# Performance work log

Hardware: AMD Instinct MI355X
Metric: run time of the kernel (lower is better)

## Reference

```python
import jax, jax.numpy as jnp
import numpy as np

NUM_TARGETS = 2
N_ITER = 20
REF_MIC = 1          # 1-based reference mic
CONTRAST = 'laplace'
GAMMA = 1.0
PROJ_BACK = 'mdp'
TOL = 1e-5
EPS_R = 1e-10
REG = 1e-6


def contrast_weights(r, func, gamma, eps_r):
    # phi(r) = g'(r) / r for the chosen contrast function
    r = jnp.maximum(r, eps_r)
    if func == 'laplace':
        return 1.0 / (2.0 * r)
    if func == 'gaussian':
        return jnp.ones_like(r)
    if func == 'power':
        return gamma * r ** (gamma - 2.0)
    raise ValueError(func)


def _iva_forward(X):
    M, T, F, _ = X.shape
    K = NUM_TARGETS
    # (M,T,F,2) real/imag -> complex (F,M,T)
    X_c = jnp.transpose(X[..., 0] + 1j * X[..., 1], (2, 0, 1))
    cdtype = X_c.dtype
    eyeM = jnp.eye(M, dtype=cdtype)
    W_hat = jnp.tile(eyeM[None], (F, 1, 1))
    W_hat = W_hat.at[:, K:, K:].set(-jnp.eye(M - K, dtype=cdtype))
    # input covariance (constant over iterations): (F,M,M)
    C = jnp.einsum('fmt,fnt->fmn', X_c, X_c.conj()) / T
    reg_eye = REG * eyeM  # broadcasts over F / (K,F)
    eps = jnp.finfo(jnp.float32).eps
    done = jnp.array(False)

    for _ in range(N_ITER):
        W_old = W_hat
        # current target estimates: (F,K,T)
        Y = jnp.einsum('fkm,fmt->fkt', W_hat[:, :K, :], X_c)
        r = jnp.sqrt(jnp.maximum((jnp.abs(Y) ** 2).sum(axis=0), EPS_R))  # (K,T)
        w_t = contrast_weights(r, CONTRAST, GAMMA, EPS_R).astype(cdtype)
        # weighted covariances: (K,F,M,M)
        V = jnp.einsum('kt,fmt,fnt->kfmn', w_t, X_c, X_c.conj()) / T
        V_reg = V + reg_eye

        Wn = W_hat
        for k in range(K):
            temp = Wn @ V_reg[k]                              # (F,M,M)
            e_k = jnp.zeros((F, M), dtype=cdtype).at[:, k].set(1.0)
            w_vec = jnp.linalg.solve(temp, e_k[..., None])[..., 0]  # (F,M)
            denom = jnp.sqrt(
                jnp.einsum('fm,fmn,fn->f', w_vec.conj(), V_reg[k], w_vec).real + EPS_R
            )
            Wn = Wn.at[:, k, :].set((w_vec / denom[:, None]).conj())
        # background block: J = solve(tmp[:, :, :K], tmp[:, :, K:])^H
        tmp = Wn[:, :K, :] @ C                                # (F,K,M)
        J = jnp.conj(jnp.swapaxes(jnp.linalg.solve(tmp[:, :, :K], tmp[:, :, K:]), 1, 2))
        Wn = Wn.at[:, K:, :K].set(J)

        rel = jnp.linalg.norm(Wn - W_old) / jnp.maximum(jnp.linalg.norm(W_old), eps)
        W_hat = jnp.where(done, W_old, Wn)  # freeze once converged (mimics break)
        done = done | (rel < TOL)

    W = W_hat[:, :K, :]
    Y = jnp.einsum('fkm,fmt->fkt', W, X_c)  # (F,K,T)
    if REF_MIC is not None and 0 < REF_MIC <= M:
        if PROJ_BACK == 'mdp':
            A = jnp.linalg.pinv(W)               # (F,M,K)
            scale = A[:, REF_MIC - 1, :]         # (F,K)
            Y = scale[:, :, None] * Y
        elif PROJ_BACK == 'scale_constraint':
            Wp = jnp.linalg.pinv(W)
            d = jnp.max(jnp.abs(Wp), axis=1)     # (F,K)
            Y = d[:, :, None].astype(cdtype) * Y
    Y_out = jnp.transpose(Y, (1, 2, 0))          # (K,T,F)
    return jnp.stack([Y_out.real, Y_out.imag], axis=-1)


def setup_inputs() -> dict:
    key = jax.random.key(0)
    X = jax.random.normal(key, (8, 2048, 513, 2), dtype=jnp.float32)
    return {"X": X}


def reference(X):
    return _iva_forward(X)
```

## Files before the change

### kernel.cpp

```cpp
#include <hip/hip_runtime.h>

#define F_ 513
#define M_ 8
#define T_ 2048
#define K_ 2
#define NITER 20
#define REGC 1e-6
#define EPSR 1e-10
#define TOLC 1e-5
#define NG 256
#define TS 4
#define UPB ((F_ + 3) / 4)

typedef double2 cd;
__device__ __forceinline__ cd cmk(double r, double i){ cd z; z.x=r; z.y=i; return z; }
__device__ __forceinline__ cd cadd(cd a, cd b){ return cmk(a.x+b.x, a.y+b.y); }
__device__ __forceinline__ cd csub(cd a, cd b){ return cmk(a.x-b.x, a.y-b.y); }
__device__ __forceinline__ cd cmul(cd a, cd b){ return cmk(a.x*b.x - a.y*b.y, a.x*b.y + a.y*b.x); }
__device__ __forceinline__ cd cconj(cd a){ return cmk(a.x, -a.y); }
__device__ __forceinline__ cd cdiv(cd a, cd b){
  double d = b.x*b.x + b.y*b.y;
  return cmk((a.x*b.x + a.y*b.y)/d, (a.y*b.x - a.x*b.y)/d);
}
__device__ __forceinline__ double cabs2(cd a){ return a.x*a.x + a.y*a.y; }
__device__ __forceinline__ cd shflc(cd v, int l){
  cd r; r.x = __shfl(v.x, l, 64); r.y = __shfl(v.y, l, 64); return r;
}
__device__ __forceinline__ cd sel8(const cd x[8], int idx){
  cd r = x[0];
  #pragma unroll
  for (int q=1;q<8;++q) if (idx==q) r = x[q];
  return r;
}

__global__ __launch_bounds__(256) void pack_kernel(const float2* __restrict__ Xin, float2* __restrict__ Xc){
  __shared__ float tr[64][65];
  __shared__ float ti[64][65];
  int f0 = blockIdx.x*64, t0 = blockIdx.y*64, m = blockIdx.z;
  for (int i = threadIdx.x; i < 64*64; i += 256){
    int tl = i >> 6, fl = i & 63;
    int f = f0 + fl;
    float2 v; v.x = 0.f; v.y = 0.f;
    if (f < F_) v = Xin[((size_t)m*T_ + (t0 + tl))*F_ + f];
    tr[tl][fl] = v.x; ti[tl][fl] = v.y;
  }
  __syncthreads();
  for (int i = threadIdx.x; i < 64*32; i += 256){
    int fl = i >> 5, tl2 = i & 31;
    int f = f0 + fl;
    if (f < F_){
      int t = 2*tl2;
      float4 v;
      v.x = tr[t][fl];   v.y = ti[t][fl];
      v.z = tr[t+1][fl]; v.w = ti[t+1][fl];
      *(float4*)&Xc[((size_t)f*8 + m)*T_ + t0 + t] = v;
    }
  }
}

__global__ __launch_bounds__(256) void winit_kernel(float2* __restrict__ W){
  int idx = blockIdx.x*256 + threadIdx.x;
  if (idx >= F_*64) return;
  int l = idx & 63; int i = l>>3, j = l&7;
  float v = (i==j) ? (i < K_ ? 1.f : -1.f) : 0.f;
  float2 o; o.x = v; o.y = 0.f;
  W[idx] = o;
}

template<int MODE>
__global__ __launch_bounds__(512, 8) void cov_kernel(const float2* __restrict__ Xc, const float2* __restrict__ wts2,
                                                     cd* __restrict__ outP, const int* __restrict__ flags){
  if (MODE == 1 && *(volatile const int*)flags) return;
  __shared__ float2 xs[8][514];
  __shared__ float2 wsm2[512];
  int f = blockIdx.x, s = blockIdx.y;
  int tid = threadIdx.x;
  int w = tid >> 6, lane = tid & 63;
  int m = lane >> 3, n = lane & 7;
  #pragma unroll
  for (int r=0; r<4; ++r){
    int idx = tid + r*512;
    int mm = idx >> 8, q = idx & 255;
    float4 v = ((const float4*)(Xc + ((size_t)f*8 + mm)*T_ + s*512))[q];
    *(float4*)&xs[mm][q*2] = v;
  }
  if (MODE == 1) wsm2[tid] = wts2[s*512 + tid];
  __syncthreads();
  const float2* xm = xs[m];
  const float2* xn = xs[n];
  int tbase = w*64;
  float a0r=0.f, a0i=0.f, a1r=0.f, a1i=0.f;
  #pragma unroll 8
  for (int tt=0; tt<64; tt+=2){
    float4 av = *(const float4*)&xm[tbase+tt];
    float4 bv = *(const float4*)&xn[tbase+tt];
    float zr0 = fmaf(av.x, bv.x, av.y*bv.y);
    float zi0 = fmaf(av.y, bv.x, -av.x*bv.y);
    float zr1 = fmaf(av.z, bv.z, av.w*bv.w);
    float zi1 = fmaf(av.w, bv.z, -av.z*bv.w);
    if (MODE == 0){
      a0r += zr0 + zr1; a0i += zi0 + zi1;
    } else {
      float4 wv = *(const float4*)&wsm2[tbase+tt];
      a0r = fmaf(wv.x, zr0, a0r); a0i = fmaf(wv.x, zi0, a0i);
      a1r = fmaf(wv.y, zr0, a1r); a1i = fmaf(wv.y, zi0, a1i);
      a0r = fmaf(wv.z, zr1, a0r); a0i = fmaf(wv.z, zi1, a0i);
      a1r = fmaf(wv.w, zr1, a1r); a1i = fmaf(wv.w, zi1, a1i);
    }
  }
  __syncthreads();
  float* wred = (float*)&xs[0][0];
  wred[0*512 + w*64 + lane] = a0r;
  wred[1*512 + w*64 + lane] = a0i;
  if (MODE == 1){
    wred[2*512 + w*64 + lane] = a1r;
    wred[3*512 + w*64 + lane] = a1i;
  }
  __syncthreads();
  const double inv = 1.0/(double)T_;
  int nk = (MODE == 0) ? 1 : 2;
  if (tid < nk*64){
    int k = tid >> 6, l = tid & 63;
    float rr = 0.f, ii = 0.f;
    #pragma unroll
    for (int ww=0; ww<8; ++ww){
      rr += wred[(k*2+0)*512 + ww*64 + l];
      ii += wred[(k*2+1)*512 + ww*64 + l];
    }
    cd o = cmk((double)rr*inv, (double)ii*inv);
    if (MODE == 0) outP[((size_t)f*TS + s)*64 + l] = o;
    else           outP[(((size_t)k*F_ + f)*TS + s)*64 + l] = o;
  }
}

__global__ __launch_bounds__(256) void yr_kernel(const float2* __restrict__ Xc, const float2* __restrict__ Wg,
                                                 float* __restrict__ part, const int* __restrict__ flags){
  if (*(volatile const int*)flags) return;
  int g = blockIdx.y;
  int t = blockIdx.x*256 + threadIdx.x;
  float acc0 = 0.f, acc1 = 0.f;
  for (int f = g; f < F_; f += NG){
    const float2* Wf = Wg + (size_t)f*64;
    float2 y0; y0.x=0; y0.y=0;
    float2 y1; y1.x=0; y1.y=0;
    #pragma unroll
    for (int m=0;m<8;++m){
      float2 xv = Xc[((size_t)f*8 + m)*T_ + t];
      float2 w0 = Wf[m];
      float2 w1 = Wf[8+m];
      y0.x = fmaf(w0.x,xv.x,fmaf(-w0.y,xv.y,y0.x)); y0.y = fmaf(w0.x,xv.y,fmaf(w0.y,xv.x,y0.y));
      y1.x = fmaf(w1.x,xv.x,fmaf(-w1.y,xv.y,y1.x)); y1.y = fmaf(w1.x,xv.y,fmaf(w1.y,xv.x,y1.y));
    }
    acc0 += y0.x*y0.x + y0.y*y0.y;
    acc1 += y1.x*y1.x + y1.y*y1.y;
  }
  part[((size_t)g*2+0)*T_ + t] = acc0;
  part[((size_t)g*2+1)*T_ + t] = acc1;
}

__global__ __launch_bounds__(256) void rw_kernel(const float* __restrict__ part, float* __restrict__ wts2f,
                                                 const int* __restrict__ flags){
  if (*(volatile const int*)flags) return;
  int v = blockIdx.x*256 + threadIdx.x;
  int k = v >> 11, t = v & (T_-1);
  double s = 0;
  for (int g=0; g<NG; ++g) s += (double)part[((size_t)g*2+k)*T_ + t];
  wts2f[2*t + k] = (float)(0.5 / sqrt(fmax(s, EPSR)));
}

__global__ __launch_bounds__(256) void update_kernel(const cd* __restrict__ Vp, const cd* __restrict__ Cp,
                                                     float2* __restrict__ Wg,
                                                     double* __restrict__ dsum, double* __restrict__ osum,
                                                     int* __restrict__ flags){
  if (*(volatile const int*)flags) return;
  int lane = threadIdx.x & 63;
  int w = threadIdx.x >> 6;
  int f = blockIdx.x*4 + w;
  int i = lane >> 3, j = lane & 7;
  double ds = 0.0, os = 0.0;
  if (f < F_){
    float2 wf = Wg[(size_t)f*64 + lane];
    cd Wn = cmk(wf.x, wf.y);
    cd Wold = Wn;
    cd x[8];
    #pragma unroll
    for (int k=0; k<K_; ++k){
      cd Vr = cmk(0,0);
      #pragma unroll
      for (int s2=0; s2<TS; ++s2)
        Vr = cadd(Vr, Vp[(((size_t)k*F_ + f)*TS + s2)*64 + lane]);
      if (i == j) Vr.x += REGC;
      cd temp = cmk(0,0);
      #pragma unroll
      for (int q=0;q<8;++q) temp = cadd(temp, cmul(shflc(Wn, i*8+q), shflc(Vr, q*8+j)));
      cd b = cmk(i==k ? 1.0 : 0.0, 0.0);
      for (int p=0; p<8; ++p){
        double pv = (j==p && i>=p) ? cabs2(temp) : -1.0;
        int pidx = i;
        for (int off=32; off; off>>=1){
          double ov = __shfl_xor(pv, off, 64);
          int oi = __shfl_xor(pidx, off, 64);
          if (ov > pv){ pv = ov; pidx = oi; }
        }
        cd tp = shflc(temp, pidx*8 + j);
        cd tq = shflc(temp, p*8 + j);
        cd bp_ = shflc(b, pidx*8 + j);
        cd bq_ = shflc(b, p*8 + j);
        if (i == p){ temp = tp; b = bp_; }
        else if (i == pidx){ temp = tq; b = bq_; }
        cd tip = shflc(temp, i*8 + p);
        cd tpp = shflc(temp, p*8 + p);
        cd tpj = shflc(temp, p*8 + j);
        cd bpr = shflc(b, p*8 + j);
        cd fac = cdiv(tip, tpp);
        if (i > p){ temp = csub(temp, cmul(fac, tpj)); b = csub(b, cmul(fac, bpr)); }
      }
      #pragma unroll
      for (int p=7; p>=0; --p){
        cd s = shflc(b, p*8);
        #pragma unroll
        for (int q=p+1; q<8; ++q){
          cd tpq = shflc(temp, p*8 + q);
          s = csub(s, cmul(tpq, x[q]));
        }
        x[p] = cdiv(s, shflc(temp, p*8 + p));
      }
      cd xi = sel8(x, i), xj = sel8(x, j);
      cd z = cmul(cconj(xi), Vr);
      double dl = z.x*xj.x - z.y*xj.y;
      for (int off=32; off; off>>=1) dl += __shfl_xor(dl, off, 64);
      double denom = sqrt(dl + EPSR);
      if (i == k){ Wn = cmk(xj.x/denom, -xj.y/denom); }
    }
    cd Cc = cmk(0,0);
    #pragma unroll
    for (int s2=0; s2<TS; ++s2)
      Cc = cadd(Cc, Cp[((size_t)f*TS + s2)*64 + lane]);
    cd tmp = cmk(0,0);
    #pragma unroll
    for (int q=0;q<8;++q) tmp = cadd(tmp, cmul(shflc(Wn, i*8+q), shflc(Cc, q*8+j)));
    cd A = shflc(tmp, 0), B = shflc(tmp, 1), C2 = shflc(tmp, 8), D = shflc(tmp, 9);
    cd det = csub(cmul(A,D), cmul(B,C2));
    cd t0 = shflc(tmp, i);
    cd t1 = shflc(tmp, 8 + i);
    cd Z0 = cdiv(csub(cmul(D,t0), cmul(B,t1)), det);
    cd Z1 = cdiv(csub(cmul(A,t1), cmul(C2,t0)), det);
    if (i >= K_ && j < K_){
      cd Z = (j==0) ? Z0 : Z1;
      Wn = cconj(Z);
    }
    ds = cabs2(csub(Wn, Wold));
    os = cabs2(Wold);
    for (int off=32; off; off>>=1){
      ds += __shfl_xor(ds, off, 64);
      os += __shfl_xor(os, off, 64);
    }
    float2 wo; wo.x = (float)Wn.x; wo.y = (float)Wn.y;
    Wg[(size_t)f*64 + lane] = wo;
  }
  __shared__ double sd[4], so[4];
  __shared__ int lastFlag;
  if (lane == 0){ sd[w] = ds; so[w] = os; }
  __syncthreads();
  if (threadIdx.x == 0){
    dsum[blockIdx.x] = sd[0]+sd[1]+sd[2]+sd[3];
    osum[blockIdx.x] = so[0]+so[1]+so[2]+so[3];
  }
  __threadfence();
  if (threadIdx.x == 0){
    int tk = atomicAdd(&flags[1], 1);
    lastFlag = (tk == UPB-1) ? 1 : 0;
  }
  __syncthreads();
  if (lastFlag && threadIdx.x < 64){
    __threadfence();
    double d=0, o=0;
    for (int idx=lane; idx<UPB; idx+=64){
      d += ((volatile double*)dsum)[idx];
      o += ((volatile double*)osum)[idx];
    }
    for (int off=32; off; off>>=1){ d += __shfl_xor(d, off, 64); o += __shfl_xor(o, off, 64); }
    if (lane == 0){
      flags[1] = 0;
      double rel = sqrt(d) / fmax(sqrt(o), 1.1920928955078125e-7);
      if (rel < TOLC) flags[0] = 1;
    }
  }
}

__global__ __launch_bounds__(256) void scale_kernel(const float2* __restrict__ Wg, float2* __restrict__ scale){
  int f = blockIdx.x*256 + threadIdx.x;
  if (f >= F_) return;
  cd w0[8], w1[8];
  #pragma unroll
  for (int m=0;m<8;++m){
    float2 a = Wg[(size_t)f*64 + m];     w0[m] = cmk(a.x, a.y);
    float2 b = Wg[(size_t)f*64 + 8 + m]; w1[m] = cmk(b.x, b.y);
  }
  cd G00 = cmk(0,0), G01 = cmk(0,0), G11 = cmk(0,0);
  #pragma unroll
  for (int m=0;m<8;++m){
    G00 = cadd(G00, cmul(w0[m], cconj(w0[m])));
    G01 = cadd(G01, cmul(w0[m], cconj(w1[m])));
    G11 = cadd(G11, cmul(w1[m], cconj(w1[m])));
  }
  cd G10 = cconj(G01);
  cd det = csub(cmul(G00,G11), cmul(G01,G10));
  cd I00 = cdiv(G11, det), I01 = cdiv(cmk(-G01.x,-G01.y), det);
  cd I10 = cdiv(cmk(-G10.x,-G10.y), det), I11 = cdiv(G00, det);
  cd c0 = cconj(w0[0]), c1 = cconj(w1[0]);
  cd s0 = cadd(cmul(c0, I00), cmul(c1, I10));
  cd s1 = cadd(cmul(c0, I01), cmul(c1, I11));
  float2 o0; o0.x=(float)s0.x; o0.y=(float)s0.y;
  float2 o1; o1.x=(float)s1.x; o1.y=(float)s1.y;
  scale[(size_t)f*2 + 0] = o0;
  scale[(size_t)f*2 + 1] = o1;
}

__global__ __launch_bounds__(256) void out_kernel(const float2* __restrict__ Xc, const float2* __restrict__ Wg,
                                                  const float2* __restrict__ scale, float2* __restrict__ out){
  __shared__ float re0[32][65], im0[32][65], re1[32][65], im1[32][65];
  int f0 = blockIdx.x*32, t0 = blockIdx.y*64;
  int lane = threadIdx.x & 63, w = threadIdx.x >> 6;
  for (int fl = w; fl < 32; fl += 4){
    int f = f0 + fl;
    if (f < F_){
      const float2* Wf = Wg + (size_t)f*64;
      int t = t0 + lane;
      float2 y0; y0.x=0; y0.y=0;
      float2 y1; y1.x=0; y1.y=0;
      #pragma unroll
      for (int m=0;m<8;++m){
        float2 xv = Xc[((size_t)f*8 + m)*T_ + t];
        float2 w0 = Wf[m];
        float2 w1 = Wf[8+m];
        y0.x += w0.x*xv.x - w0.y*xv.y; y0.y += w0.x*xv.y + w0.y*xv.x;
        y1.x += w1.x*xv.x - w1.y*xv.y; y1.y += w1.x*xv.y + w1.y*xv.x;
      }
      float2 s0 = scale[(size_t)f*2 + 0];
      float2 s1 = scale[(size_t)f*2 + 1];
      re0[fl][lane] = s0.x*y0.x - s0.y*y0.y; im0[fl][lane] = s0.x*y0.y + s0.y*y0.x;
      re1[fl][lane] = s1.x*y1.x - s1.y*y1.y; im1[fl][lane] = s1.x*y1.y + s1.y*y1.x;
    }
  }
  __syncthreads();
  for (int i = threadIdx.x; i < 32*64; i += 256){
    int tl = i >> 5, fl = i & 31;
    int f = f0 + fl;
    if (f < F_){
      int t = t0 + tl;
      float2 o0; o0.x = re0[fl][tl]; o0.y = im0[fl][tl];
      float2 o1; o1.x = re1[fl][tl]; o1.y = im1[fl][tl];
      out[((size_t)(0*T_ + t))*F_ + f] = o0;
      out[((size_t)(1*T_ + t))*F_ + f] = o1;
    }
  }
}

extern "C" void kernel_launch(void* const* d_in, const int* in_sizes, int n_in,
                              void* d_out, int out_size, void* d_ws, size_t ws_size,
                              hipStream_t stream) {
  const float2* Xin = (const float2*)d_in[0];
  char* ws = (char*)d_ws;
  size_t off = 0;
  auto alloc = [&](size_t bytes) -> void* {
    void* p = ws + off;
    off += (bytes + 255) & ~(size_t)255;
    return p;
  };
  float2* Xc   = (float2*)alloc((size_t)F_*M_*T_*8);
  cd*     Cp   = (cd*)alloc((size_t)F_*TS*64*16);
  cd*     Vp   = (cd*)alloc((size_t)K_*F_*TS*64*16);
  float2* W    = (float2*)alloc((size_t)F_*64*8);
  float*  part = (float*)alloc((size_t)NG*K_*T_*4);
  float2* wts2 = (float2*)alloc((size_t)T_*8);
  double* dsum = (double*)alloc((size_t)UPB*8);
  double* osum = (double*)alloc((size_t)UPB*8);
  float2* sc   = (float2*)alloc((size_t)F_*K_*8);
  int*    flags= (int*)alloc(256);
  if (off > ws_size) return;

  hipMemsetAsync(flags, 0, 12, stream);

  pack_kernel<<<dim3(9, 32, 8), 256, 0, stream>>>(Xin, Xc);
  winit_kernel<<<(F_*64 + 255)/256, 256, 0, stream>>>(W);
  cov_kernel<0><<<dim3(F_, TS), 512, 0, stream>>>(Xc, nullptr, Cp, flags);

  for (int it=0; it<NITER; ++it){
    yr_kernel<<<dim3(T_/256, NG), 256, 0, stream>>>(Xc, W, part, flags);
    rw_kernel<<<(K_*T_ + 255)/256, 256, 0, stream>>>(part, (float*)wts2, flags);
    cov_kernel<1><<<dim3(F_, TS), 512, 0, stream>>>(Xc, wts2, Vp, flags);
    update_kernel<<<UPB, 256, 0, stream>>>(Vp, Cp, W, dsum, osum, flags);
  }

  scale_kernel<<<(F_ + 255)/256, 256, 0, stream>>>(W, sc);
  out_kernel<<<dim3(17, 32), 256, 0, stream>>>(Xc, W, sc, (float2*)d_out);
}
```

Measured before the change: 1.670 ms.

## Fuse weighted covariance, W update and next Y-power into one per-frequency kernel

Merges the weighted covariance, the per-frequency demixing update and the next iteration's |Y|^2 computation into a single kernel with one block per frequency. This cuts the loop from four launches to two and drops the global Vp round trip. The first iteration's power is taken from cov0 because W starts as identity. The rw reduction now sums per-frequency partials over 513 entries instead of 256 groups, and the pack tile height is halved. The cost is that only 513 blocks loop serially over time segments, so parallelism falls, and one wave does the solve while the others wait.

```diff
diff --git a/kernel.cpp b/kernel.cpp
--- a/kernel.cpp
+++ b/kernel.cpp
@@ -8,9 +8,7 @@
 #define REGC 1e-6
 #define EPSR 1e-10
 #define TOLC 1e-5
-#define NG 256
 #define TS 4
-#define UPB ((F_ + 3) / 4)
 
 typedef double2 cd;
 __device__ __forceinline__ cd cmk(double r, double i){ cd z; z.x=r; z.y=i; return z; }
@@ -34,10 +32,10 @@
 }
 
 __global__ __launch_bounds__(256) void pack_kernel(const float2* __restrict__ Xin, float2* __restrict__ Xc){
-  __shared__ float tr[64][65];
-  __shared__ float ti[64][65];
-  int f0 = blockIdx.x*64, t0 = blockIdx.y*64, m = blockIdx.z;
-  for (int i = threadIdx.x; i < 64*64; i += 256){
+  __shared__ float tr[32][65];
+  __shared__ float ti[32][65];
+  int f0 = blockIdx.x*64, t0 = blockIdx.y*32, m = blockIdx.z;
+  for (int i = threadIdx.x; i < 32*64; i += 256){
     int tl = i >> 6, fl = i & 63;
     int f = f0 + fl;
     float2 v; v.x = 0.f; v.y = 0.f;
@@ -45,8 +43,8 @@
     tr[tl][fl] = v.x; ti[tl][fl] = v.y;
   }
   __syncthreads();
-  for (int i = threadIdx.x; i < 64*32; i += 256){
-    int fl = i >> 5, tl2 = i & 31;
+  for (int i = threadIdx.x; i < 64*16; i += 256){
+    int fl = i >> 4, tl2 = i & 15;
     int f = f0 + fl;
     if (f < F_){
       int t = 2*tl2;
@@ -67,12 +65,10 @@
   W[idx] = o;
 }
 
-template<int MODE>
-__global__ __launch_bounds__(512, 8) void cov_kernel(const float2* __restrict__ Xc, const float2* __restrict__ wts2,
-                                                     cd* __restrict__ outP, const int* __restrict__ flags){
-  if (MODE == 1 && *(volatile const int*)flags) return;
+__global__ __launch_bounds__(512) void cov0_kernel(const float2* __restrict__ Xc, cd* __restrict__ Cp,
+                                                   float2* __restrict__ part){
   __shared__ float2 xs[8][514];
-  __shared__ float2 wsm2[512];
+  __shared__ double wred[2][8][64];
   int f = blockIdx.x, s = blockIdx.y;
   int tid = threadIdx.x;
   int w = tid >> 6, lane = tid & 63;
@@ -84,111 +80,135 @@
     float4 v = ((const float4*)(Xc + ((size_t)f*8 + mm)*T_ + s*512))[q];
     *(float4*)&xs[mm][q*2] = v;
   }
-  if (MODE == 1) wsm2[tid] = wts2[s*512 + tid];
-  __syncthreads();
+  __syncthreads();
+  {
+    float2 x0 = xs[0][tid], x1 = xs[1][tid];
+    part[(size_t)f*T_ + s*512 + tid] =
+      make_float2(fmaf(x0.x,x0.x,x0.y*x0.y), fmaf(x1.x,x1.x,x1.y*x1.y));
+  }
   const float2* xm = xs[m];
   const float2* xn = xs[n];
   int tbase = w*64;
-  float a0r=0.f, a0i=0.f, a1r=0.f, a1i=0.f;
+  float ar=0.f, ai=0.f;
   #pragma unroll 8
   for (int tt=0; tt<64; tt+=2){
     float4 av = *(const float4*)&xm[tbase+tt];
     float4 bv = *(const float4*)&xn[tbase+tt];
-    float zr0 = fmaf(av.x, bv.x, av.y*bv.y);
-    float zi0 = fmaf(av.y, bv.x, -av.x*bv.y);
-    float zr1 = fmaf(av.z, bv.z, av.w*bv.w);
-    float zi1 = fmaf(av.w, bv.z, -av.z*bv.w);
-    if (MODE == 0){
-      a0r += zr0 + zr1; a0i += zi0 + zi1;
-    } else {
+    ar += fmaf(av.x, bv.x, av.y*bv.y) + fmaf(av.z, bv.z, av.w*bv.w);
+    ai += fmaf(av.y, bv.x, -av.x*bv.y) + fmaf(av.w, bv.z, -av.z*bv.w);
+  }
+  wred[0][w][lane] = ar; wred[1][w][lane] = ai;
+  __syncthreads();
+  if (tid < 64){
+    double sr=0, si=0;
+    #pragma unroll
+    for (int ww=0; ww<8; ++ww){ sr += wred[0][ww][tid]; si += wred[1][ww][tid]; }
+    const double inv = 1.0/(double)T_;
+    Cp[((size_t)f*TS + s)*64 + tid] = cmk(sr*inv, si*inv);
+  }
+}
+
+__global__ __launch_bounds__(512) void rw_kernel(const float2* __restrict__ part, float2* __restrict__ wts2,
+                                                 const int* __restrict__ flags){
+  if (*(volatile const int*)flags) return;
+  __shared__ double wred[8][64][2];
+  int tid = threadIdx.x;
+  int w = tid >> 6, lane = tid & 63;
+  int t = blockIdx.x*64 + lane;
+  double s0=0, s1=0;
+  for (int f=w; f<F_; f+=8){
+    float2 p = part[(size_t)f*T_ + t];
+    s0 += (double)p.x; s1 += (double)p.y;
+  }
+  wred[w][lane][0]=s0; wred[w][lane][1]=s1;
+  __syncthreads();
+  if (tid < 64){
+    double a=0,b=0;
+    #pragma unroll
+    for (int ww=0; ww<8; ++ww){ a += wred[ww][tid][0]; b += wred[ww][tid][1]; }
+    wts2[blockIdx.x*64 + tid] =
+      make_float2((float)(0.5/sqrt(fmax(a,EPSR))), (float)(0.5/sqrt(fmax(b,EPSR))));
+  }
+}
+
+__global__ __launch_bounds__(512, 4) void covupd_kernel(
+    const float2* __restrict__ Xc, const float2* __restrict__ wts2,
+    const cd* __restrict__ Cp, float2* __restrict__ Wg,
+    float2* __restrict__ part, double* __restrict__ dsum, double* __restrict__ osum,
+    int* __restrict__ flags, int do_yr)
+{
+  if (*(volatile const int*)flags) return;
+  __shared__ float2 xs[8][514];
+  __shared__ float2 wsm2[512];
+  __shared__ double wred[4][8][64];
+  __shared__ double Vd[2][64][2];
+  __shared__ cd Cl[64];
+  __shared__ cd Wl[64];
+  __shared__ int lastF;
+  int f = blockIdx.x;
+  int tid = threadIdx.x;
+  int w = tid >> 6, lane = tid & 63;
+  int m = lane >> 3, n = lane & 7;
+  double va0r=0, va0i=0, va1r=0, va1i=0;
+  for (int s=0; s<TS; ++s){
+    if (s) __syncthreads();
+    #pragma unroll
+    for (int r=0; r<4; ++r){
+      int idx = tid + r*512;
+      int mm = idx >> 8, q = idx & 255;
+      float4 v = ((const float4*)(Xc + ((size_t)f*8 + mm)*T_ + s*512))[q];
+      *(float4*)&xs[mm][q*2] = v;
+    }
+    wsm2[tid] = wts2[s*512 + tid];
+    __syncthreads();
+    const float2* xm = xs[m];
+    const float2* xn = xs[n];
+    int tbase = w*64;
+    float a0r=0.f, a0i=0.f, a1r=0.f, a1i=0.f;
+    #pragma unroll 8
+    for (int tt=0; tt<64; tt+=2){
+      float4 av = *(const float4*)&xm[tbase+tt];
+      float4 bv = *(const float4*)&xn[tbase+tt];
+      float zr0 = fmaf(av.x, bv.x, av.y*bv.y);
+      float zi0 = fmaf(av.y, bv.x, -av.x*bv.y);
+      float zr1 = fmaf(av.z, bv.z, av.w*bv.w);
+      float zi1 = fmaf(av.w, bv.z, -av.z*bv.w);
       float4 wv = *(const float4*)&wsm2[tbase+tt];
       a0r = fmaf(wv.x, zr0, a0r); a0i = fmaf(wv.x, zi0, a0i);
       a1r = fmaf(wv.y, zr0, a1r); a1i = fmaf(wv.y, zi0, a1i);
       a0r = fmaf(wv.z, zr1, a0r); a0i = fmaf(wv.z, zi1, a0i);
       a1r = fmaf(wv.w, zr1, a1r); a1i = fmaf(wv.w, zi1, a1i);
     }
-  }
-  __syncthreads();
-  float* wred = (float*)&xs[0][0];
-  wred[0*512 + w*64 + lane] = a0r;
-  wred[1*512 + w*64 + lane] = a0i;
-  if (MODE == 1){
-    wred[2*512 + w*64 + lane] = a1r;
-    wred[3*512 + w*64 + lane] = a1i;
-  }
-  __syncthreads();
-  const double inv = 1.0/(double)T_;
-  int nk = (MODE == 0) ? 1 : 2;
-  if (tid < nk*64){
-    int k = tid >> 6, l = tid & 63;
-    float rr = 0.f, ii = 0.f;
-    #pragma unroll
-    for (int ww=0; ww<8; ++ww){
-      rr += wred[(k*2+0)*512 + ww*64 + l];
-      ii += wred[(k*2+1)*512 + ww*64 + l];
-    }
-    cd o = cmk((double)rr*inv, (double)ii*inv);
-    if (MODE == 0) outP[((size_t)f*TS + s)*64 + l] = o;
-    else           outP[(((size_t)k*F_ + f)*TS + s)*64 + l] = o;
-  }
-}
-
-__global__ __launch_bounds__(256) void yr_kernel(const float2* __restrict__ Xc, const float2* __restrict__ Wg,
-                                                 float* __restrict__ part, const int* __restrict__ flags){
-  if (*(volatile const int*)flags) return;
-  int g = blockIdx.y;
-  int t = blockIdx.x*256 + threadIdx.x;
-  float acc0 = 0.f, acc1 = 0.f;
-  for (int f = g; f < F_; f += NG){
-    const float2* Wf = Wg + (size_t)f*64;
-    float2 y0; y0.x=0; y0.y=0;
-    float2 y1; y1.x=0; y1.y=0;
-    #pragma unroll
-    for (int m=0;m<8;++m){
-      float2 xv = Xc[((size_t)f*8 + m)*T_ + t];
-      float2 w0 = Wf[m];
-      float2 w1 = Wf[8+m];
-      y0.x = fmaf(w0.x,xv.x,fmaf(-w0.y,xv.y,y0.x)); y0.y = fmaf(w0.x,xv.y,fmaf(w0.y,xv.x,y0.y));
-      y1.x = fmaf(w1.x,xv.x,fmaf(-w1.y,xv.y,y1.x)); y1.y = fmaf(w1.x,xv.y,fmaf(w1.y,xv.x,y1.y));
-    }
-    acc0 += y0.x*y0.x + y0.y*y0.y;
-    acc1 += y1.x*y1.x + y1.y*y1.y;
-  }
-  part[((size_t)g*2+0)*T_ + t] = acc0;
-  part[((size_t)g*2+1)*T_ + t] = acc1;
-}
-
-__global__ __launch_bounds__(256) void rw_kernel(const float* __restrict__ part, float* __restrict__ wts2f,
-                                                 const int* __restrict__ flags){
-  if (*(volatile const int*)flags) return;
-  int v = blockIdx.x*256 + threadIdx.x;
-  int k = v >> 11, t = v & (T_-1);
-  double s = 0;
-  for (int g=0; g<NG; ++g) s += (double)part[((size_t)g*2+k)*T_ + t];
-  wts2f[2*t + k] = (float)(0.5 / sqrt(fmax(s, EPSR)));
-}
-
-__global__ __launch_bounds__(256) void update_kernel(const cd* __restrict__ Vp, const cd* __restrict__ Cp,
-                                                     float2* __restrict__ Wg,
-                                                     double* __restrict__ dsum, double* __restrict__ osum,
-                                                     int* __restrict__ flags){
-  if (*(volatile const int*)flags) return;
-  int lane = threadIdx.x & 63;
-  int w = threadIdx.x >> 6;
-  int f = blockIdx.x*4 + w;
-  int i = lane >> 3, j = lane & 7;
-  double ds = 0.0, os = 0.0;
-  if (f < F_){
+    va0r += a0r; va0i += a0i; va1r += a1r; va1i += a1i;
+  }
+  wred[0][w][lane] = va0r;
+  wred[1][w][lane] = va0i;
+  wred[2][w][lane] = va1r;
+  wred[3][w][lane] = va1i;
+  __syncthreads();
+  if (tid < 256){
+    int q = tid >> 6, l = tid & 63;
+    double ssum = 0;
+    #pragma unroll
+    for (int ww=0; ww<8; ++ww) ssum += wred[q][ww][l];
+    Vd[q>>1][l][q&1] = ssum * (1.0/(double)T_);
+  } else if (tid < 320){
+    int l = tid - 256;
+    cd c = cmk(0,0);
+    #pragma unroll
+    for (int s2=0; s2<TS; ++s2) c = cadd(c, Cp[((size_t)f*TS + s2)*64 + l]);
+    Cl[l] = c;
+  }
+  __syncthreads();
+  if (w == 0){
+    int i = lane >> 3, j = lane & 7;
     float2 wf = Wg[(size_t)f*64 + lane];
     cd Wn = cmk(wf.x, wf.y);
     cd Wold = Wn;
     cd x[8];
     #pragma unroll
     for (int k=0; k<K_; ++k){
-      cd Vr = cmk(0,0);
-      #pragma unroll
-      for (int s2=0; s2<TS; ++s2)
-        Vr = cadd(Vr, Vp[(((size_t)k*F_ + f)*TS + s2)*64 + lane]);
+      cd Vr = cmk(Vd[k][lane][0], Vd[k][lane][1]);
       if (i == j) Vr.x += REGC;
       cd temp = cmk(0,0);
       #pragma unroll
@@ -232,10 +252,7 @@
       double denom = sqrt(dl + EPSR);
       if (i == k){ Wn = cmk(xj.x/denom, -xj.y/denom); }
     }
-    cd Cc = cmk(0,0);
-    #pragma unroll
-    for (int s2=0; s2<TS; ++s2)
-      Cc = cadd(Cc, Cp[((size_t)f*TS + s2)*64 + lane]);
+    cd Cc = Cl[lane];
     cd tmp = cmk(0,0);
     #pragma unroll
     for (int q=0;q<8;++q) tmp = cadd(tmp, cmul(shflc(Wn, i*8+q), shflc(Cc, q*8+j)));
@@ -249,38 +266,68 @@
       cd Z = (j==0) ? Z0 : Z1;
       Wn = cconj(Z);
     }
-    ds = cabs2(csub(Wn, Wold));
-    os = cabs2(Wold);
+    double ds = cabs2(csub(Wn, Wold));
+    double os = cabs2(Wold);
     for (int off=32; off; off>>=1){
       ds += __shfl_xor(ds, off, 64);
       os += __shfl_xor(os, off, 64);
     }
+    Wl[lane] = Wn;
     float2 wo; wo.x = (float)Wn.x; wo.y = (float)Wn.y;
     Wg[(size_t)f*64 + lane] = wo;
-  }
-  __shared__ double sd[4], so[4];
-  __shared__ int lastFlag;
-  if (lane == 0){ sd[w] = ds; so[w] = os; }
-  __syncthreads();
-  if (threadIdx.x == 0){
-    dsum[blockIdx.x] = sd[0]+sd[1]+sd[2]+sd[3];
-    osum[blockIdx.x] = so[0]+so[1]+so[2]+so[3];
+    if (lane == 0){ dsum[f] = ds; osum[f] = os; }
+  } else if (do_yr){
+    for (int idx = tid - 64; idx < 2048; idx += 448){
+      int mm = idx >> 8, q = idx & 255;
+      float4 v = ((const float4*)(Xc + ((size_t)f*8 + mm)*T_))[q];
+      *(float4*)&xs[mm][q*2] = v;
+    }
+  }
+  __syncthreads();
+  if (do_yr){
+    float2 w0f[8], w1f[8];
+    #pragma unroll
+    for (int mm=0;mm<8;++mm){
+      cd c0 = Wl[mm], c1 = Wl[8+mm];
+      w0f[mm] = make_float2((float)c0.x, (float)c0.y);
+      w1f[mm] = make_float2((float)c1.x, (float)c1.y);
+    }
+    for (int s=0; s<TS; ++s){
+      if (s){
+        __syncthreads();
+        #pragma unroll
+        for (int r=0; r<4; ++r){
+          int idx = tid + r*512;
+          int mm = idx >> 8, q = idx & 255;
+          float4 v = ((const float4*)(Xc + ((size_t)f*8 + mm)*T_ + s*512))[q];
+          *(float4*)&xs[mm][q*2] = v;
+        }
+        __syncthreads();
+      }
+      float2 y0 = make_float2(0.f,0.f), y1 = make_float2(0.f,0.f);
+      #pragma unroll
+      for (int mm=0;mm<8;++mm){
+        float2 xv = xs[mm][tid];
+        float2 a = w0f[mm], b = w1f[mm];
+        y0.x = fmaf(a.x,xv.x,fmaf(-a.y,xv.y,y0.x)); y0.y = fmaf(a.x,xv.y,fmaf(a.y,xv.x,y0.y));
+        y1.x = fmaf(b.x,xv.x,fmaf(-b.y,xv.y,y1.x)); y1.y = fmaf(b.x,xv.y,fmaf(b.y,xv.x,y1.y));
+      }
+      part[(size_t)f*T_ + s*512 + tid] =
+        make_float2(fmaf(y0.x,y0.x,y0.y*y0.y), fmaf(y1.x,y1.x,y1.y*y1.y));
+    }
   }
   __threadfence();
-  if (threadIdx.x == 0){
-    int tk = atomicAdd(&flags[1], 1);
-    lastFlag = (tk == UPB-1) ? 1 : 0;
-  }
-  __syncthreads();
-  if (lastFlag && threadIdx.x < 64){
+  if (tid == 0) lastF = (atomicAdd(&flags[1], 1) == F_-1) ? 1 : 0;
+  __syncthreads();
+  if (lastF && tid < 64){
     __threadfence();
     double d=0, o=0;
-    for (int idx=lane; idx<UPB; idx+=64){
+    for (int idx=tid; idx<F_; idx+=64){
       d += ((volatile double*)dsum)[idx];
       o += ((volatile double*)osum)[idx];
     }
     for (int off=32; off; off>>=1){ d += __shfl_xor(d, off, 64); o += __shfl_xor(o, off, 64); }
-    if (lane == 0){
+    if (tid == 0){
       flags[1] = 0;
       double rel = sqrt(d) / fmax(sqrt(o), 1.1920928955078125e-7);
       if (rel < TOLC) flags[0] = 1;
@@ -370,27 +417,25 @@
   };
   float2* Xc   = (float2*)alloc((size_t)F_*M_*T_*8);
   cd*     Cp   = (cd*)alloc((size_t)F_*TS*64*16);
-  cd*     Vp   = (cd*)alloc((size_t)K_*F_*TS*64*16);
   float2* W    = (float2*)alloc((size_t)F_*64*8);
-  float*  part = (float*)alloc((size_t)NG*K_*T_*4);
+  float2* part = (float2*)alloc((size_t)F_*T_*8);
   float2* wts2 = (float2*)alloc((size_t)T_*8);
-  double* dsum = (double*)alloc((size_t)UPB*8);
-  double* osum = (double*)alloc((size_t)UPB*8);
+  double* dsum = (double*)alloc((size_t)F_*8);
+  double* osum = (double*)alloc((size_t)F_*8);
   float2* sc   = (float2*)alloc((size_t)F_*K_*8);
   int*    flags= (int*)alloc(256);
   if (off > ws_size) return;
 
   hipMemsetAsync(flags, 0, 12, stream);
 
-  pack_kernel<<<dim3(9, 32, 8), 256, 0, stream>>>(Xin, Xc);
+  pack_kernel<<<dim3(9, 64, 8), 256, 0, stream>>>(Xin, Xc);
   winit_kernel<<<(F_*64 + 255)/256, 256, 0, stream>>>(W);
-  cov_kernel<0><<<dim3(F_, TS), 512, 0, stream>>>(Xc, nullptr, Cp, flags);
+  cov0_kernel<<<dim3(F_, TS), 512, 0, stream>>>(Xc, Cp, part);
 
   for (int it=0; it<NITER; ++it){
-    yr_kernel<<<dim3(T_/256, NG), 256, 0, stream>>>(Xc, W, part, flags);
-    rw_kernel<<<(K_*T_ + 255)/256, 256, 0, stream>>>(part, (float*)wts2, flags);
-    cov_kernel<1><<<dim3(F_, TS), 512, 0, stream>>>(Xc, wts2, Vp, flags);
-    update_kernel<<<UPB, 256, 0, stream>>>(Vp, Cp, W, dsum, osum, flags);
+    rw_kernel<<<32, 512, 0, stream>>>(part, wts2, flags);
+    covupd_kernel<<<F_, 512, 0, stream>>>(Xc, wts2, Cp, W, part, dsum, osum, flags,
+                                          (it < NITER-1) ? 1 : 0);
   }
 
   scale_kernel<<<(F_ + 255)/256, 256, 0, stream>>>(W, sc);
```

New measurement: 3.656 ms. +118.9%, slower.
